# Optimization experiments

Hardware: AMD Instinct MI355X
Metric: run time of the kernel (lower is better)

## Reference

```python
import jax, jax.numpy as jnp
import numpy as np

H = 128  # hidden_size

def setup_inputs() -> dict:
    key = jax.random.key(0)
    ks = jax.random.split(key, 12)
    B, SEQ = 256, 1000
    static = jax.random.normal(ks[0], (B, 2, SEQ), jnp.float32)
    dynamic = jax.random.uniform(ks[1], (B, 2, SEQ), jnp.float32)
    # Encoder = 1x1 Conv1d(in_ch -> H): weight (H, in_ch), bias (H,)
    def xavier(k, shape):
        fan_in, fan_out = shape[1], shape[0]
        lim = np.sqrt(6.0 / (fan_in + fan_out)).astype(np.float32)
        return jax.random.uniform(k, shape, jnp.float32, -lim, lim)
    enc_s_w = xavier(ks[2], (H, 2)); enc_s_b = jnp.zeros((H,), jnp.float32)
    enc_d_w = xavier(ks[3], (H, 2)); enc_d_b = jnp.zeros((H,), jnp.float32)
    v = xavier(ks[4], (1, H))[0]                 # attention vector (H,)
    W = xavier(ks[5], (H, 3 * H))                # attention matrix (H, 3H)
    dense_w = xavier(ks[6], (H, 128)); dense_b = jnp.zeros((H,), jnp.float32)
    lin_w = xavier(ks[7], (1, H)); lin_b = jnp.zeros((1,), jnp.float32)
    return {"static": static, "dynamic": dynamic,
            "enc_s_w": enc_s_w, "enc_s_b": enc_s_b,
            "enc_d_w": enc_d_w, "enc_d_b": enc_d_b,
            "v": v, "W": W,
            "dense_w": dense_w, "dense_b": dense_b,
            "lin_w": lin_w, "lin_b": lin_b}


def reference(static, dynamic, enc_s_w, enc_s_b, enc_d_w, enc_d_b,
              v, W, dense_w, dense_b, lin_w, lin_b):
    B = static.shape[0]
    # 1x1-conv encoders (computed once; identical across loop iterations)
    e = jnp.einsum('hc,bcs->bhs', enc_s_w, static) + enc_s_b[None, :, None]   # (B,H,S)
    dyn_ld = jnp.broadcast_to(dynamic[:, 1:2, :], dynamic.shape)              # load channel expanded
    d = jnp.einsum('hc,bcs->bhs', enc_d_w, dyn_ld) + enc_d_b[None, :, None]   # (B,H,S)
    hy = jnp.zeros((B, H), static.dtype)
    for _ in range(3):  # fixed 3-step refinement loop
        hidden = jnp.concatenate(
            [e, d, jnp.broadcast_to(hy[:, :, None], e.shape)], axis=1)        # (B,3H,S)
        u = jnp.tanh(jnp.einsum('hk,bks->bhs', W, hidden))                    # (B,H,S)
        logit = jnp.einsum('h,bhs->bs', v, u)                                 # (B,S)
        prob = jax.nn.softmax(logit, axis=-1)
        hy = jnp.einsum('bs,bhs->bh', prob, e)                                # context update
    out = jax.nn.relu(hy @ dense_w.T + dense_b) @ lin_w.T + lin_b             # (B,1)
    return out
```

## Files before the change

### kernel.cpp

```cpp
#include <hip/hip_runtime.h>
#include <math.h>

#define HH 128
#define SS 1000
#define NT 1024
#define NW (NT / 64)

#define C1 2.8853900817779268f
#define C2 1.4426950408889634f

__global__ void sc_precompute(const float* __restrict__ enc_s_w,
                              const float* __restrict__ enc_s_b,
                              const float* __restrict__ enc_d_w,
                              const float* __restrict__ enc_d_b,
                              const float* __restrict__ v,
                              const float* __restrict__ W,
                              float* __restrict__ ws) {
    int h = threadIdx.x;
    if (h < HH) {
        const float* Wr = W + h * (3 * HH);
        float a0 = 0.f, a1 = 0.f, ad = 0.f, cc = 0.f, w30 = 0.f, w31 = 0.f, w3b = 0.f;
        for (int k = 0; k < HH; ++k) {
            float w1 = Wr[k], w2 = Wr[HH + k], w3 = Wr[2 * HH + k];
            a0  = fmaf(w1, enc_s_w[2 * k + 0], a0);
            a1  = fmaf(w1, enc_s_w[2 * k + 1], a1);
            ad  = fmaf(w2, enc_d_w[2 * k + 0] + enc_d_w[2 * k + 1], ad);
            cc  = fmaf(w1, enc_s_b[k], cc);
            cc  = fmaf(w2, enc_d_b[k], cc);
            w30 = fmaf(w3, enc_s_w[2 * k + 0], w30);
            w31 = fmaf(w3, enc_s_w[2 * k + 1], w31);
            w3b = fmaf(w3, enc_s_b[k], w3b);
        }
        ws[h]           = a0 * C1;
        ws[HH + h]      = a1 * C1;
        ws[2 * HH + h]  = ad * C1;
        ws[3 * HH + h]  = v[h];
        ws[4 * HH + h]  = cc * C1;
        ws[5 * HH + h]  = w30 * C1;
        ws[6 * HH + h]  = w31 * C1;
        ws[7 * HH + h]  = w3b * C1;
    }
    __syncthreads();
    if (h == 0) {
        float s = 0.f;
        for (int k = 0; k < HH; ++k) s += v[k];
        ws[8 * HH] = s * C2;
    }
}

__global__ __launch_bounds__(NT) void sc_main(
    const float* __restrict__ stat, const float* __restrict__ dyn,
    const float* __restrict__ ws,
    const float* __restrict__ enc_s_w, const float* __restrict__ enc_s_b,
    const float* __restrict__ dense_w, const float* __restrict__ dense_b,
    const float* __restrict__ lin_w, const float* __restrict__ lin_b,
    float* __restrict__ out) {
    const int b    = blockIdx.x;
    const int t    = threadIdx.x;
    const int wave = t >> 6;
    const int lane = t & 63;

    __shared__ __align__(16) float kc[4 * HH];
    __shared__ __align__(16) float cgs[HH];
    __shared__ float4 red4[NW];
    __shared__ float hy_sh[HH];

    if (t < 4 * HH) kc[t] = ws[t];

    const float* ccs = ws + 4 * HH;
    const float* w30 = ws + 5 * HH;
    const float* w31 = ws + 6 * HH;
    const float* w3b = ws + 7 * HH;
    const float  svc2 = ws[8 * HH];

    const bool valid = (t < SS);
    float x0 = 0.f, x1 = 0.f, yv = 0.f;
    if (valid) {
        const float* sb = stat + (size_t)b * 2 * SS;
        x0 = sb[t];
        x1 = sb[SS + t];
        yv = dyn[(size_t)b * 2 * SS + SS + t];
    }

    float X0 = 0.f, X1 = 0.f;

    for (int iter = 0; iter < 3; ++iter) {
        if (t < HH) {
            float g = ccs[t];
            if (iter > 0) g += fmaf(w30[t], X0, fmaf(w31[t], X1, w3b[t]));
            cgs[t] = g;
        }
        __syncthreads();

        float acc = 0.f;
        const float4* A0 = (const float4*)kc;
        const float4* A1 = (const float4*)(kc + HH);
        const float4* AD = (const float4*)(kc + 2 * HH);
        const float4* VV = (const float4*)(kc + 3 * HH);
        const float4* CG = (const float4*)cgs;
        #pragma unroll 4
        for (int j = 0; j < HH / 4; ++j) {
            float4 a0 = A0[j], a1 = A1[j], ad = AD[j], vv = VV[j], cg = CG[j];
            float z0 = fmaf(a0.x, x0, fmaf(a1.x, x1, fmaf(ad.x, yv, cg.x)));
            float z1 = fmaf(a0.y, x0, fmaf(a1.y, x1, fmaf(ad.y, yv, cg.y)));
            float z2 = fmaf(a0.z, x0, fmaf(a1.z, x1, fmaf(ad.z, yv, cg.z)));
            float z3 = fmaf(a0.w, x0, fmaf(a1.w, x1, fmaf(ad.w, yv, cg.w)));
            float e0 = __builtin_amdgcn_exp2f(z0);
            float e1 = __builtin_amdgcn_exp2f(z1);
            float e2 = __builtin_amdgcn_exp2f(z2);
            float e3 = __builtin_amdgcn_exp2f(z3);
            float r0 = __builtin_amdgcn_rcpf(1.f + e0);
            float r1 = __builtin_amdgcn_rcpf(1.f + e1);
            float r2 = __builtin_amdgcn_rcpf(1.f + e2);
            float r3 = __builtin_amdgcn_rcpf(1.f + e3);
            acc = fmaf(vv.x, r0, acc);
            acc = fmaf(vv.y, r1, acc);
            acc = fmaf(vv.z, r2, acc);
            acc = fmaf(vv.w, r3, acc);
        }

        float p = valid ? __builtin_amdgcn_exp2f(fmaf(-C1, acc, svc2)) : 0.f;

        float s0 = p, s1 = p * x0, s2 = p * x1;
        #pragma unroll
        for (int off = 32; off > 0; off >>= 1) {
            s0 += __shfl_xor(s0, off);
            s1 += __shfl_xor(s1, off);
            s2 += __shfl_xor(s2, off);
        }
        if (lane == 0) red4[wave] = make_float4(s0, s1, s2, 0.f);
        __syncthreads();

        float4 w4 = red4[lane & 15];
        #pragma unroll
        for (int off = 1; off < 16; off <<= 1) {
            w4.x += __shfl_xor(w4.x, off);
            w4.y += __shfl_xor(w4.y, off);
            w4.z += __shfl_xor(w4.z, off);
        }
        float inv = __builtin_amdgcn_rcpf(w4.x);
        X0 = w4.y * inv;
        X1 = w4.z * inv;
    }

    if (t < HH)
        hy_sh[t] = fmaf(enc_s_w[2 * t], X0, fmaf(enc_s_w[2 * t + 1], X1, enc_s_b[t]));
    __syncthreads();

    float o = 0.f;
    if (t < HH) {
        const float* dw = dense_w + t * HH;
        float r = dense_b[t];
        #pragma unroll 8
        for (int h = 0; h < HH; ++h) r = fmaf(dw[h], hy_sh[h], r);
        o = lin_w[t] * fmaxf(r, 0.f);
    }
    #pragma unroll
    for (int off = 32; off > 0; off >>= 1) o += __shfl_xor(o, off);
    if (lane == 0) red4[wave].x = o;
    __syncthreads();
    if (t == 0) {
        float s = 0.f;
        for (int i = 0; i < NW; ++i) s += red4[i].x;
        out[b] = s + lin_b[0];
    }
}

extern "C" void kernel_launch(void* const* d_in, const int* in_sizes, int n_in,
                              void* d_out, int out_size, void* d_ws, size_t ws_size,
                              hipStream_t stream) {
    const float* stat    = (const float*)d_in[0];
    const float* dyn     = (const float*)d_in[1];
    const float* enc_s_w = (const float*)d_in[2];
    const float* enc_s_b = (const float*)d_in[3];
    const float* enc_d_w = (const float*)d_in[4];
    const float* enc_d_b = (const float*)d_in[5];
    const float* v       = (const float*)d_in[6];
    const float* W       = (const float*)d_in[7];
    const float* dense_w = (const float*)d_in[8];
    const float* dense_b = (const float*)d_in[9];
    const float* lin_w   = (const float*)d_in[10];
    const float* lin_b   = (const float*)d_in[11];
    float* out = (float*)d_out;
    float* ws  = (float*)d_ws;

    const int B = in_sizes[0] / (2 * SS);

    hipLaunchKernelGGL(sc_precompute, dim3(1), dim3(HH), 0, stream,
                       enc_s_w, enc_s_b, enc_d_w, enc_d_b, v, W, ws);
    hipLaunchKernelGGL(sc_main, dim3(B), dim3(NT), 0, stream,
                       stat, dyn, ws, enc_s_w, enc_s_b, dense_w, dense_b,
                       lin_w, lin_b, out);
}
```

Baseline: 46.52 us.

## Read folded attention coefficients from global via uniform loads, drop per-iteration LDS staging

The main kernel no longer copies the precomputed coefficient tables into shared memory or builds a per-iteration bias array. The sigmoid-accumulate loop now reads the tables straight from the workspace with wave-uniform addresses, which the compiler can turn into scalar loads. The iteration bias is folded in on the fly from a pre-summed table, which removes one barrier per iteration. The reduction buffer is double-buffered to avoid a write-after-read hazard, and the precompute and dense layers are vectorized with float4 loads. The trade-off is extra FMAs per element in iterations two and three, and a reliance on scalar-cache hits instead of LDS broadcast.

```diff
diff --git a/kernel.cpp b/kernel.cpp
--- a/kernel.cpp
+++ b/kernel.cpp
@@ -17,35 +17,97 @@
                               const float* __restrict__ W,
                               float* __restrict__ ws) {
     int h = threadIdx.x;
-    if (h < HH) {
-        const float* Wr = W + h * (3 * HH);
-        float a0 = 0.f, a1 = 0.f, ad = 0.f, cc = 0.f, w30 = 0.f, w31 = 0.f, w3b = 0.f;
-        for (int k = 0; k < HH; ++k) {
-            float w1 = Wr[k], w2 = Wr[HH + k], w3 = Wr[2 * HH + k];
-            a0  = fmaf(w1, enc_s_w[2 * k + 0], a0);
-            a1  = fmaf(w1, enc_s_w[2 * k + 1], a1);
-            ad  = fmaf(w2, enc_d_w[2 * k + 0] + enc_d_w[2 * k + 1], ad);
-            cc  = fmaf(w1, enc_s_b[k], cc);
-            cc  = fmaf(w2, enc_d_b[k], cc);
-            w30 = fmaf(w3, enc_s_w[2 * k + 0], w30);
-            w31 = fmaf(w3, enc_s_w[2 * k + 1], w31);
-            w3b = fmaf(w3, enc_s_b[k], w3b);
-        }
-        ws[h]           = a0 * C1;
-        ws[HH + h]      = a1 * C1;
-        ws[2 * HH + h]  = ad * C1;
-        ws[3 * HH + h]  = v[h];
-        ws[4 * HH + h]  = cc * C1;
-        ws[5 * HH + h]  = w30 * C1;
-        ws[6 * HH + h]  = w31 * C1;
-        ws[7 * HH + h]  = w3b * C1;
-    }
-    __syncthreads();
+    if (h >= HH) return;
+    const float4* W1 = (const float4*)(W + h * (3 * HH));
+    const float4* W2 = (const float4*)(W + h * (3 * HH) + HH);
+    const float4* W3 = (const float4*)(W + h * (3 * HH) + 2 * HH);
+    const float4* ES = (const float4*)enc_s_w;
+    const float4* ED = (const float4*)enc_d_w;
+    const float4* SB = (const float4*)enc_s_b;
+    const float4* DB = (const float4*)enc_d_b;
+    float a0 = 0.f, a1 = 0.f, ad = 0.f, cc = 0.f, w30 = 0.f, w31 = 0.f, w3b = 0.f;
+    #pragma unroll 4
+    for (int k4 = 0; k4 < HH / 4; ++k4) {
+        float4 w1 = W1[k4], w2 = W2[k4], w3 = W3[k4];
+        float4 e01 = ES[2 * k4], e23 = ES[2 * k4 + 1];
+        float4 d01 = ED[2 * k4], d23 = ED[2 * k4 + 1];
+        float4 sb = SB[k4], db = DB[k4];
+        a0 = fmaf(w1.x, e01.x, a0); a0 = fmaf(w1.y, e01.z, a0);
+        a0 = fmaf(w1.z, e23.x, a0); a0 = fmaf(w1.w, e23.z, a0);
+        a1 = fmaf(w1.x, e01.y, a1); a1 = fmaf(w1.y, e01.w, a1);
+        a1 = fmaf(w1.z, e23.y, a1); a1 = fmaf(w1.w, e23.w, a1);
+        ad = fmaf(w2.x, d01.x + d01.y, ad); ad = fmaf(w2.y, d01.z + d01.w, ad);
+        ad = fmaf(w2.z, d23.x + d23.y, ad); ad = fmaf(w2.w, d23.z + d23.w, ad);
+        cc = fmaf(w1.x, sb.x, cc); cc = fmaf(w1.y, sb.y, cc);
+        cc = fmaf(w1.z, sb.z, cc); cc = fmaf(w1.w, sb.w, cc);
+        cc = fmaf(w2.x, db.x, cc); cc = fmaf(w2.y, db.y, cc);
+        cc = fmaf(w2.z, db.z, cc); cc = fmaf(w2.w, db.w, cc);
+        w30 = fmaf(w3.x, e01.x, w30); w30 = fmaf(w3.y, e01.z, w30);
+        w30 = fmaf(w3.z, e23.x, w30); w30 = fmaf(w3.w, e23.z, w30);
+        w31 = fmaf(w3.x, e01.y, w31); w31 = fmaf(w3.y, e01.w, w31);
+        w31 = fmaf(w3.z, e23.y, w31); w31 = fmaf(w3.w, e23.w, w31);
+        w3b = fmaf(w3.x, sb.x, w3b); w3b = fmaf(w3.y, sb.y, w3b);
+        w3b = fmaf(w3.z, sb.z, w3b); w3b = fmaf(w3.w, sb.w, w3b);
+    }
+    ws[h]            = a0 * C1;
+    ws[HH + h]       = a1 * C1;
+    ws[2 * HH + h]   = ad * C1;
+    ws[3 * HH + h]   = v[h];
+    ws[4 * HH + h]   = cc * C1;
+    ws[5 * HH + h]   = (cc + w3b) * C1;
+    ws[6 * HH + h]   = w30 * C1;
+    ws[7 * HH + h]   = w31 * C1;
     if (h == 0) {
+        const float4* V4 = (const float4*)v;
         float s = 0.f;
-        for (int k = 0; k < HH; ++k) s += v[k];
+        #pragma unroll 4
+        for (int k = 0; k < HH / 4; ++k) { float4 t = V4[k]; s += t.x + t.y + t.z + t.w; }
         ws[8 * HH] = s * C2;
     }
+}
+
+template <bool FIRST>
+__device__ __forceinline__ float sig_acc(const float* __restrict__ ws,
+                                         float x0, float x1, float yv,
+                                         float X0, float X1) {
+    const float4* A0 = (const float4*)(ws);
+    const float4* A1 = (const float4*)(ws + HH);
+    const float4* AD = (const float4*)(ws + 2 * HH);
+    const float4* VV = (const float4*)(ws + 3 * HH);
+    const float4* CC = (const float4*)(ws + (FIRST ? 4 * HH : 5 * HH));
+    const float4* W0 = (const float4*)(ws + 6 * HH);
+    const float4* W1 = (const float4*)(ws + 7 * HH);
+    float acc = 0.f;
+    #pragma unroll 2
+    for (int j = 0; j < HH / 4; ++j) {
+        float4 cg = CC[j];
+        float b0 = cg.x, b1 = cg.y, b2 = cg.z, b3 = cg.w;
+        if (!FIRST) {
+            float4 w0 = W0[j], w1 = W1[j];
+            b0 = fmaf(w0.x, X0, fmaf(w1.x, X1, b0));
+            b1 = fmaf(w0.y, X0, fmaf(w1.y, X1, b1));
+            b2 = fmaf(w0.z, X0, fmaf(w1.z, X1, b2));
+            b3 = fmaf(w0.w, X0, fmaf(w1.w, X1, b3));
+        }
+        float4 a0 = A0[j], a1 = A1[j], ad = AD[j], vv = VV[j];
+        float z0 = fmaf(a0.x, x0, fmaf(a1.x, x1, fmaf(ad.x, yv, b0)));
+        float z1 = fmaf(a0.y, x0, fmaf(a1.y, x1, fmaf(ad.y, yv, b1)));
+        float z2 = fmaf(a0.z, x0, fmaf(a1.z, x1, fmaf(ad.z, yv, b2)));
+        float z3 = fmaf(a0.w, x0, fmaf(a1.w, x1, fmaf(ad.w, yv, b3)));
+        float e0 = __builtin_amdgcn_exp2f(z0);
+        float e1 = __builtin_amdgcn_exp2f(z1);
+        float e2 = __builtin_amdgcn_exp2f(z2);
+        float e3 = __builtin_amdgcn_exp2f(z3);
+        float r0 = __builtin_amdgcn_rcpf(1.f + e0);
+        float r1 = __builtin_amdgcn_rcpf(1.f + e1);
+        float r2 = __builtin_amdgcn_rcpf(1.f + e2);
+        float r3 = __builtin_amdgcn_rcpf(1.f + e3);
+        acc = fmaf(vv.x, r0, acc);
+        acc = fmaf(vv.y, r1, acc);
+        acc = fmaf(vv.z, r2, acc);
+        acc = fmaf(vv.w, r3, acc);
+    }
+    return acc;
 }
 
 __global__ __launch_bounds__(NT) void sc_main(
@@ -60,18 +122,10 @@
     const int wave = t >> 6;
     const int lane = t & 63;
 
-    __shared__ __align__(16) float kc[4 * HH];
-    __shared__ __align__(16) float cgs[HH];
-    __shared__ float4 red4[NW];
-    __shared__ float hy_sh[HH];
-
-    if (t < 4 * HH) kc[t] = ws[t];
-
-    const float* ccs = ws + 4 * HH;
-    const float* w30 = ws + 5 * HH;
-    const float* w31 = ws + 6 * HH;
-    const float* w3b = ws + 7 * HH;
-    const float  svc2 = ws[8 * HH];
+    __shared__ float4 red4[2][NW];
+    __shared__ __align__(16) float hy_sh[HH];
+
+    const float svc2 = ws[8 * HH];
 
     const bool valid = (t < SS);
     float x0 = 0.f, x1 = 0.f, yv = 0.f;
@@ -84,43 +138,8 @@
 
     float X0 = 0.f, X1 = 0.f;
 
-    for (int iter = 0; iter < 3; ++iter) {
-        if (t < HH) {
-            float g = ccs[t];
-            if (iter > 0) g += fmaf(w30[t], X0, fmaf(w31[t], X1, w3b[t]));
-            cgs[t] = g;
-        }
-        __syncthreads();
-
-        float acc = 0.f;
-        const float4* A0 = (const float4*)kc;
-        const float4* A1 = (const float4*)(kc + HH);
-        const float4* AD = (const float4*)(kc + 2 * HH);
-        const float4* VV = (const float4*)(kc + 3 * HH);
-        const float4* CG = (const float4*)cgs;
-        #pragma unroll 4
-        for (int j = 0; j < HH / 4; ++j) {
-            float4 a0 = A0[j], a1 = A1[j], ad = AD[j], vv = VV[j], cg = CG[j];
-            float z0 = fmaf(a0.x, x0, fmaf(a1.x, x1, fmaf(ad.x, yv, cg.x)));
-            float z1 = fmaf(a0.y, x0, fmaf(a1.y, x1, fmaf(ad.y, yv, cg.y)));
-            float z2 = fmaf(a0.z, x0, fmaf(a1.z, x1, fmaf(ad.z, yv, cg.z)));
-            float z3 = fmaf(a0.w, x0, fmaf(a1.w, x1, fmaf(ad.w, yv, cg.w)));
-            float e0 = __builtin_amdgcn_exp2f(z0);
-            float e1 = __builtin_amdgcn_exp2f(z1);
-            float e2 = __builtin_amdgcn_exp2f(z2);
-            float e3 = __builtin_amdgcn_exp2f(z3);
-            float r0 = __builtin_amdgcn_rcpf(1.f + e0);
-            float r1 = __builtin_amdgcn_rcpf(1.f + e1);
-            float r2 = __builtin_amdgcn_rcpf(1.f + e2);
-            float r3 = __builtin_amdgcn_rcpf(1.f + e3);
-            acc = fmaf(vv.x, r0, acc);
-            acc = fmaf(vv.y, r1, acc);
-            acc = fmaf(vv.z, r2, acc);
-            acc = fmaf(vv.w, r3, acc);
-        }
-
+    auto reduce3 = [&](float acc, int parity) {
         float p = valid ? __builtin_amdgcn_exp2f(fmaf(-C1, acc, svc2)) : 0.f;
-
         float s0 = p, s1 = p * x0, s2 = p * x1;
         #pragma unroll
         for (int off = 32; off > 0; off >>= 1) {
@@ -128,10 +147,9 @@
             s1 += __shfl_xor(s1, off);
             s2 += __shfl_xor(s2, off);
         }
-        if (lane == 0) red4[wave] = make_float4(s0, s1, s2, 0.f);
+        if (lane == 0) red4[parity][wave] = make_float4(s0, s1, s2, 0.f);
         __syncthreads();
-
-        float4 w4 = red4[lane & 15];
+        float4 w4 = red4[parity][lane & 15];
         #pragma unroll
         for (int off = 1; off < 16; off <<= 1) {
             w4.x += __shfl_xor(w4.x, off);
@@ -141,7 +159,11 @@
         float inv = __builtin_amdgcn_rcpf(w4.x);
         X0 = w4.y * inv;
         X1 = w4.z * inv;
-    }
+    };
+
+    reduce3(sig_acc<true>(ws, x0, x1, yv, 0.f, 0.f), 0);
+    reduce3(sig_acc<false>(ws, x0, x1, yv, X0, X1), 1);
+    reduce3(sig_acc<false>(ws, x0, x1, yv, X0, X1), 0);
 
     if (t < HH)
         hy_sh[t] = fmaf(enc_s_w[2 * t], X0, fmaf(enc_s_w[2 * t + 1], X1, enc_s_b[t]));
@@ -149,19 +171,23 @@
 
     float o = 0.f;
     if (t < HH) {
-        const float* dw = dense_w + t * HH;
+        const float4* dw4 = (const float4*)(dense_w + t * HH);
+        const float4* hy4 = (const float4*)hy_sh;
         float r = dense_b[t];
-        #pragma unroll 8
-        for (int h = 0; h < HH; ++h) r = fmaf(dw[h], hy_sh[h], r);
+        #pragma unroll 4
+        for (int k = 0; k < HH / 4; ++k) {
+            float4 d4 = dw4[k], h4 = hy4[k];
+            r = fmaf(d4.x, h4.x, fmaf(d4.y, h4.y, fmaf(d4.z, h4.z, fmaf(d4.w, h4.w, r))));
+        }
         o = lin_w[t] * fmaxf(r, 0.f);
     }
     #pragma unroll
     for (int off = 32; off > 0; off >>= 1) o += __shfl_xor(o, off);
-    if (lane == 0) red4[wave].x = o;
+    if (lane == 0) red4[0][wave].x = o;
     __syncthreads();
     if (t == 0) {
         float s = 0.f;
-        for (int i = 0; i < NW; ++i) s += red4[i].x;
+        for (int i = 0; i < NW; ++i) s += red4[0][i].x;
         out[b] = s + lin_b[0];
     }
 }
```

Result: slower. 51.30 us (+10.3%).
